# Performance work log

Measured on AMD Instinct MI355X. Metric: run time of the kernel, lower is better.

## Reference

```python
import jax, jax.numpy as jnp
import numpy as np

N_NODES = 100000
N_EDGES = 800000
DIM = 128
BN_EPS = 1e-5


def setup_inputs() -> dict:
    key = jax.random.key(0)
    k1, k2, k3 = jax.random.split(key, 3)
    x = jax.random.normal(k1, (N_NODES, DIM), dtype=jnp.float32)
    edge_index = jax.random.randint(k2, (2, N_EDGES), 0, N_NODES, dtype=jnp.int64)
    # xavier-uniform-like init for the linear weight [out, in]
    limit = float(np.sqrt(6.0 / (DIM + DIM)))
    W = jax.random.uniform(k3, (DIM, DIM), dtype=jnp.float32, minval=-limit, maxval=limit)
    bias = jnp.zeros((DIM,), dtype=jnp.float32)
    bn_gamma = jnp.ones((DIM,), dtype=jnp.float32)
    bn_beta = jnp.zeros((DIM,), dtype=jnp.float32)
    return {"x": x, "edge_index": edge_index, "W": W, "bias": bias,
            "bn_gamma": bn_gamma, "bn_beta": bn_beta, "bit_sum": 0}


def reference(x, edge_index, W, bias, bn_gamma, bn_beta, bit_sum):
    n = x.shape[0]
    # Linear (no bias), is_q=False path; q_xw treated as identity.
    h = x @ W.T                                   # [N, D]
    row, col = edge_index[0], edge_index[1]
    # symmetric degree normalization: deg computed over destination (col)
    deg = jax.ops.segment_sum(jnp.ones_like(col, dtype=h.dtype), col, num_segments=n)
    deg_inv_sqrt = jnp.where(deg > 0, jax.lax.rsqrt(jnp.maximum(deg, 1.0)), 0.0)
    norm = deg_inv_sqrt[row] * deg_inv_sqrt[col]  # [E]
    # message: norm * x_j (x_j = h[row]), aggregate (add) at col
    msg = norm[:, None] * h[row]                  # [E, D]
    out = jax.ops.segment_sum(msg, col, num_segments=n)  # [N, D]
    out = out + bias
    # BatchNorm1d (training mode: batch stats, biased variance)
    mean = jnp.mean(out, axis=0)
    var = jnp.var(out, axis=0)
    out = (out - mean) * jax.lax.rsqrt(var + BN_EPS) * bn_gamma + bn_beta
    # activation
    out = jax.nn.relu(out)
    # residual (in_dim == out_dim); dropout p=0 -> identity
    out = out + x
    return (out, 0)
```

## Files before the change

### kernel.cpp

```cpp
#include <hip/hip_runtime.h>
#include <cstddef>

#define NN 100000
#define DD 128
#define ND (NN * DD)
#define BN_EPS 1e-5f
#define LDA 136
#define NREP 16
#define NBKT 98
#define EPB 4096
#define NT ((NN + 63) / 64)

typedef __bf16 bf16_t;
typedef bf16_t bf16x8 __attribute__((ext_vector_type(8)));
typedef float f32x4 __attribute__((ext_vector_type(4)));
typedef unsigned int uint;
typedef unsigned short ushort;


__device__ __forceinline__ ushort f2b(float f) {
    uint u = __builtin_bit_cast(uint, f);
    u += 0x7FFFu + ((u >> 16) & 1u);
    return (ushort)(u >> 16);
}
__device__ __forceinline__ float b2f(uint s) {
    return __builtin_bit_cast(float, s << 16);
}
__device__ __forceinline__ float blo(uint u) {
    return __builtin_bit_cast(float, u << 16);
}
__device__ __forceinline__ float bhi(uint u) {
    return __builtin_bit_cast(float, u & 0xFFFF0000u);
}

__device__ __forceinline__ int detect_i64(const int* __restrict__ ei) {
    __shared__ int sflag;
    int t = threadIdx.x;
    if (t < 64) {
        int hi = ei[2 * t + 1];
        unsigned long long b = __ballot(hi == 0);
        if (t == 0) sflag = (b == ~0ull) ? 1 : 0;
    }
    __syncthreads();
    return sflag;
}

__global__ __launch_bounds__(256) void k_prep(const int* __restrict__ ei,
                                              int* __restrict__ bktot, int E, int nbh,
                                              const float* __restrict__ x,
                                              uint* __restrict__ xb,
                                              const float* __restrict__ W,
                                              uint* __restrict__ wb) {
    if ((int)blockIdx.x < nbh) {
        int f = detect_i64(ei);
        __shared__ int hist[NBKT];
        int t = threadIdx.x;
        if (t < NBKT) hist[t] = 0;
        __syncthreads();
        int base = blockIdx.x * EPB;
        int count = min(EPB, E - base);
        for (int i = t; i < count; i += 256) {
            int e = base + i;
            int c = f ? ei[2 * (E + e)] : ei[E + e];
            atomicAdd(&hist[c >> 10], 1);
        }
        __syncthreads();
        if (t < NBKT && hist[t] > 0) atomicAdd(&bktot[t], hist[t]);
        return;
    }
    int i = (blockIdx.x - nbh) * 256 + threadIdx.x;
    const float* src;
    uint* dst;
    int j;
    if (i < ND / 8) { src = x; dst = xb; j = i; }
    else { j = i - ND / 8; if (j >= (DD * DD) / 8) return; src = W; dst = wb; }
    const float4* s4 = (const float4*)src;
    float4 a = s4[2 * j], b = s4[2 * j + 1];
    uint4 o;
    o.x = (uint)f2b(a.x) | ((uint)f2b(a.y) << 16);
    o.y = (uint)f2b(a.z) | ((uint)f2b(a.w) << 16);
    o.z = (uint)f2b(b.x) | ((uint)f2b(b.y) << 16);
    o.w = (uint)f2b(b.z) | ((uint)f2b(b.w) << 16);
    ((uint4*)dst)[j] = o;
}

__global__ __launch_bounds__(256) void k_bin(const int* __restrict__ ei,
                                             const int* __restrict__ bktot,
                                             int* __restrict__ bcur,
                                             uint2* __restrict__ pairs, int E) {
    int f = detect_i64(ei);
    __shared__ int bb[NBKT], hist[NBKT], scur[NBKT];
    int t = threadIdx.x;
    if (t < NBKT) { bb[t] = bktot[t]; hist[t] = 0; }
    __syncthreads();
    if (t == 0) {
        int run = 0;
        for (int i = 0; i < NBKT; ++i) { int v = bb[i]; bb[i] = run; run += v; }
    }
    int base = blockIdx.x * EPB;
    int count = min(EPB, E - base);
    int rr[16], cc[16];
#pragma unroll
    for (int k = 0; k < 16; ++k) {
        int i = t + k * 256;
        if (i < count) {
            int e = base + i;
            int r, c;
            if (f) { r = ei[2 * e]; c = ei[2 * (E + e)]; }
            else   { r = ei[e];     c = ei[E + e]; }
            rr[k] = r; cc[k] = c;
            atomicAdd(&hist[c >> 10], 1);
        }
    }
    __syncthreads();
    if (t < NBKT) scur[t] = bb[t] + atomicAdd(&bcur[t], hist[t]);
    __syncthreads();
#pragma unroll
    for (int k = 0; k < 16; ++k) {
        int i = t + k * 256;
        if (i < count) {
            int b = cc[k] >> 10;
            int pos = atomicAdd(&scur[b], 1);
            pairs[pos] = (uint2){(uint)rr[k], (uint)cc[k]};
        }
    }
}

__global__ __launch_bounds__(256) void k_cnt(const uint2* __restrict__ pairs,
                                             const int* __restrict__ bktot,
                                             int* __restrict__ ptr0,
                                             int* __restrict__ cnt,
                                             float* __restrict__ dinv,
                                             int* __restrict__ srow) {
    __shared__ int hist[1024];
    __shared__ int scur[1024];
    __shared__ int ls[256];
    __shared__ int bb[NBKT];
    __shared__ int se0, se1;
    int b = blockIdx.x;
    int t = threadIdx.x;
    if (t < NBKT) bb[t] = bktot[t];
#pragma unroll
    for (int i = 0; i < 4; ++i) hist[t + i * 256] = 0;
    __syncthreads();
    if (t == 0) {
        int run = 0;
        for (int i = 0; i < b; ++i) run += bb[i];
        se0 = run; se1 = run + bb[b];
    }
    __syncthreads();
    int e0 = se0, e1 = se1;
    int nodebase = b << 10;
    for (int i = e0 + t; i < e1; i += 256)
        atomicAdd(&hist[(int)pairs[i].y - nodebase], 1);
    __syncthreads();
    int c4[4];
    int lsum = 0;
#pragma unroll
    for (int i = 0; i < 4; ++i) { c4[i] = hist[t * 4 + i]; lsum += c4[i]; }
    ls[t] = lsum;
    __syncthreads();
    for (int o = 1; o < 256; o <<= 1) {
        int v = (t >= o) ? ls[t - o] : 0;
        __syncthreads();
        ls[t] += v;
        __syncthreads();
    }
    int run = ls[t] - lsum + e0;
#pragma unroll
    for (int i = 0; i < 4; ++i) {
        int idx = nodebase + t * 4 + i;
        if (idx < NN) {
            ptr0[idx] = run;
            cnt[idx] = c4[i];
            dinv[idx] = c4[i] > 0 ? rsqrtf((float)c4[i]) : 0.f;
        }
        scur[t * 4 + i] = run;
        run += c4[i];
    }
    __syncthreads();
    for (int i = e0 + t; i < e1; i += 256) {
        uint2 p = pairs[i];
        int pos = atomicAdd(&scur[(int)p.y - nodebase], 1);
        srow[pos] = (int)p.x;
    }
}

__global__ __launch_bounds__(512, 4) void k_gg(const uint* __restrict__ xb,
                                               const int* __restrict__ srow,
                                               const int* __restrict__ ptr0,
                                               const int* __restrict__ cnt,
                                               const float* __restrict__ dinv,
                                               const ushort* __restrict__ wb,
                                               ushort* __restrict__ hb,
                                               float* __restrict__ csr,
                                               float* __restrict__ cqr) {
    __shared__ ushort sA[64 * LDA];
    __shared__ float cp[8][64], cq[8][64];
    int t = threadIdx.x;
    int wave = t >> 6, lane = t & 63;
    int quad = lane >> 4, l16 = lane & 15;
    uint rowbase = (uint)blockIdx.x * 64;
    const uint4* xb4 = (const uint4*)xb;

    int mn = (int)rowbase + wave * 8 + (lane & 7);
    int sv = 0, kv = 0;
    float dv = 0.f;
    if (lane < 8 && mn < NN) { sv = ptr0[mn]; kv = cnt[mn]; dv = dinv[mn]; }

    for (int bt = 0; bt < 2; ++bt) {
        int ni = bt * 4 + quad;
        int s_here = __shfl(sv, ni);
        int k_here = __shfl(kv, ni);
        float d_here = __shfl(dv, ni);
        int km = max(k_here, __shfl_xor(k_here, 16));
        km = max(km, __shfl_xor(km, 32));

        float ax0 = 0.f, ax1 = 0.f, ax2 = 0.f, ax3 = 0.f;
        float ax4 = 0.f, ax5 = 0.f, ax6 = 0.f, ax7 = 0.f;

        for (int base = 0; base < km; base += 16) {
            int rem = k_here - base;
            int rj = 0;
            if (l16 < rem) rj = srow[s_here + base + l16];
            int jend = km - base; jend = jend > 16 ? 16 : jend;
            for (int j = 0; j < jend; j += 4) {
#pragma unroll
                for (int u = 0; u < 4; ++u) {
                    int jj = j + u;
                    int rsel = __shfl(rj, (lane & 48) + jj);
                    float w = dinv[rsel];
                    uint4 v = xb4[((uint)rsel << 4) + (uint)l16];
                    w = (jj < rem) ? w : 0.f;
                    ax0 = fmaf(w, blo(v.x), ax0); ax1 = fmaf(w, bhi(v.x), ax1);
                    ax2 = fmaf(w, blo(v.y), ax2); ax3 = fmaf(w, bhi(v.y), ax3);
                    ax4 = fmaf(w, blo(v.z), ax4); ax5 = fmaf(w, bhi(v.z), ax5);
                    ax6 = fmaf(w, blo(v.w), ax6); ax7 = fmaf(w, bhi(v.w), ax7);
                }
            }
        }
        uint4 o;
        o.x = (uint)f2b(d_here * ax0) | ((uint)f2b(d_here * ax1) << 16);
        o.y = (uint)f2b(d_here * ax2) | ((uint)f2b(d_here * ax3) << 16);
        o.z = (uint)f2b(d_here * ax4) | ((uint)f2b(d_here * ax5) << 16);
        o.w = (uint)f2b(d_here * ax6) | ((uint)f2b(d_here * ax7) << 16);
        *(uint4*)(sA + (wave * 8 + ni) * LDA + l16 * 8) = o;
    }
    __syncthreads();

    int rg = wave & 3, chh = wave >> 2;
    bf16x8 Af[4];
#pragma unroll
    for (int ks = 0; ks < 4; ++ks)
        Af[ks] = __builtin_bit_cast(
            bf16x8, *(const uint4*)(sA + (rg * 16 + l16) * LDA + ks * 32 + quad * 8));

#pragma unroll
    for (int c = 0; c < 4; ++c) {
        int ctg = chh * 4 + c;
        bf16x8 Bf[4];
#pragma unroll
        for (int ks = 0; ks < 4; ++ks)
            Bf[ks] = __builtin_bit_cast(
                bf16x8,
                *(const uint4*)(wb + (uint)(ctg * 16 + l16) * 128 + ks * 32 + quad * 8));
        f32x4 acc = (f32x4){0.f, 0.f, 0.f, 0.f};
#pragma unroll
        for (int ks = 0; ks < 4; ++ks)
            acc = __builtin_amdgcn_mfma_f32_16x16x32_bf16(Af[ks], Bf[ks], acc, 0, 0, 0);
        float ss = 0.f, qq = 0.f;
#pragma unroll
        for (int r = 0; r < 4; ++r) {
            float v = acc[r];
            ss += v; qq += v * v;
            uint row = rowbase + rg * 16 + quad * 4 + r;
            if (row < NN) hb[row * 128u + (uint)(ctg * 16 + l16)] = f2b(v);
        }
        ss += __shfl_xor(ss, 16); ss += __shfl_xor(ss, 32);
        qq += __shfl_xor(qq, 16); qq += __shfl_xor(qq, 32);
        if (quad == 0) { cp[wave][c * 16 + l16] = ss; cq[wave][c * 16 + l16] = qq; }
    }
    __syncthreads();
    if (t < 128) {
        int w0 = (t >> 6) * 4, lc = t & 63;
        float s = cp[w0][lc] + cp[w0 + 1][lc] + cp[w0 + 2][lc] + cp[w0 + 3][lc];
        float q = cq[w0][lc] + cq[w0 + 1][lc] + cq[w0 + 2][lc] + cq[w0 + 3][lc];
        int rep = ((int)blockIdx.x & (NREP - 1)) * 128 + t;
        atomicAdd(&csr[rep], s);
        atomicAdd(&cqr[rep], q);
    }
}

__global__ __launch_bounds__(256) void k_final(const uint* __restrict__ hb,
                                               const uint* __restrict__ xb,
                                               const float* __restrict__ gamma,
                                               const float* __restrict__ beta,
                                               const float* __restrict__ csr,
                                               const float* __restrict__ cqr,
                                               float* __restrict__ out, int out_size) {
    __shared__ float sa[128], sb[128];
    int t = threadIdx.x;
    const float invN = 1.0f / NN;
    if (t < 128) {
        float s = 0.f;
        for (int i = 0; i < NREP; ++i) s += csr[i * 128 + t];
        sa[t] = s * invN;
    } else {
        int c = t - 128;
        float s = 0.f;
        for (int i = 0; i < NREP; ++i) s += cqr[i * 128 + c];
        sb[c] = s * invN;
    }
    __syncthreads();
    if (t < 128) {
        float m = sa[t];
        float var = sb[t] - m * m;
        float inv = rsqrtf(var + BN_EPS);
        float A = inv * gamma[t];
        float B = beta[t] - m * A;
        sa[t] = A; sb[t] = B;
    }
    __syncthreads();

    int c0 = (t & 7) * 16;
    int u8 = blockIdx.x * 512 + t * 2;
    uint4 hv0 = ((const uint4*)hb)[u8], hv1 = ((const uint4*)hb)[u8 + 1];
    uint4 xv0 = ((const uint4*)xb)[u8], xv1 = ((const uint4*)xb)[u8 + 1];
    uint hu[8] = {hv0.x, hv0.y, hv0.z, hv0.w, hv1.x, hv1.y, hv1.z, hv1.w};
    uint xu[8] = {xv0.x, xv0.y, xv0.z, xv0.w, xv1.x, xv1.y, xv1.z, xv1.w};
    float res[16];
#pragma unroll
    for (int p = 0; p < 8; ++p) {
        int c = c0 + p * 2;
        float h0 = blo(hu[p]), h1 = bhi(hu[p]);
        float x0 = blo(xu[p]), x1 = bhi(xu[p]);
        res[2 * p]     = fmaxf(fmaf(h0, sa[c],     sb[c]),     0.f) + x0;
        res[2 * p + 1] = fmaxf(fmaf(h1, sa[c + 1], sb[c + 1]), 0.f) + x1;
    }
    float4* o4 = (float4*)out;
    int ob = blockIdx.x * 1024 + t * 4;
#pragma unroll
    for (int q = 0; q < 4; ++q)
        o4[ob + q] = (float4){res[4 * q], res[4 * q + 1], res[4 * q + 2], res[4 * q + 3]};
    if (blockIdx.x == 0 && t == 0 && out_size > ND) out[ND] = 0.0f;
}

extern "C" void kernel_launch(void* const* d_in, const int* in_sizes, int n_in,
                              void* d_out, int out_size, void* d_ws, size_t ws_size,
                              hipStream_t stream) {
    const float* x     = (const float*)d_in[0];
    const int*   ei    = (const int*)d_in[1];
    const float* W     = (const float*)d_in[2];
    const float* gamma = (const float*)d_in[4];
    const float* beta  = (const float*)d_in[5];
    float* ws = (float*)d_ws;
    float* out = (float*)d_out;

    uint*   region0  = (uint*)ws;
    uint*   xb       = region0 + ND / 2;
    float*  csr      = (float*)(xb + ND / 2);
    float*  cqr      = csr + NREP * 128;
    int*    bktot    = (int*)(cqr + NREP * 128);
    int*    bcur     = bktot + 128;
    int*    cnt      = bcur + 128;
    int*    ptr0     = cnt + NN;
    float*  dinv     = (float*)(ptr0 + NN);
    int*    srow     = (int*)(dinv + NN);

    int E = in_sizes[1] / 2;
    uint* wb = (uint*)(srow + E);
    uint2* pairs = (uint2*)region0;

    int nbc = (ND / 8 + (DD * DD) / 8 + 255) / 256;
    int nbin = (E + EPB - 1) / EPB;

    hipMemsetAsync(csr, 0, (size_t)(2 * NREP * 128 + 256) * 4, stream);
    k_prep<<<nbin + nbc, 256, 0, stream>>>(ei, bktot, E, nbin, x, xb, W, wb);
    k_bin<<<nbin, 256, 0, stream>>>(ei, bktot, bcur, pairs, E);
    k_cnt<<<NBKT, 256, 0, stream>>>(pairs, bktot, ptr0, cnt, dinv, srow);
    k_gg<<<NT, 512, 0, stream>>>(xb, srow, ptr0, cnt, dinv, (const ushort*)wb,
                                 (ushort*)region0, csr, cqr);
    k_final<<<ND / 4096, 256, 0, stream>>>(region0, xb, gamma, beta, csr, cqr,
                                           out, out_size);
}
```

Measured before the change: 224.0 us.

## Use finer destination buckets and dynamic per-wave node gather in aggregation

Bucket width drops from 1024 to 256 nodes, giving 392 buckets so the counting-sort kernel launches four times as many blocks with one node per thread. The gather stage now has each wave claim whole destination nodes from a shared-memory counter, reading 4 bytes per lane across the full 128-wide row. Edge weights are prefetched per lane and passed by shuffle. The aim is better load balance across waves and more parallelism in the CSR build, at the cost of narrower per-lane loads and an LDS atomic per node.

```diff
diff --git a/kernel.cpp b/kernel.cpp
--- a/kernel.cpp
+++ b/kernel.cpp
@@ -7,7 +7,8 @@
 #define BN_EPS 1e-5f
 #define LDA 136
 #define NREP 16
-#define NBKT 98
+#define NBKT 392
+#define BSH 8
 #define EPB 4096
 #define NT ((NN + 63) / 64)
 
@@ -55,17 +56,18 @@
         int f = detect_i64(ei);
         __shared__ int hist[NBKT];
         int t = threadIdx.x;
-        if (t < NBKT) hist[t] = 0;
+        for (int i = t; i < NBKT; i += 256) hist[i] = 0;
         __syncthreads();
         int base = blockIdx.x * EPB;
         int count = min(EPB, E - base);
         for (int i = t; i < count; i += 256) {
             int e = base + i;
             int c = f ? ei[2 * (E + e)] : ei[E + e];
-            atomicAdd(&hist[c >> 10], 1);
+            atomicAdd(&hist[c >> BSH], 1);
         }
         __syncthreads();
-        if (t < NBKT && hist[t] > 0) atomicAdd(&bktot[t], hist[t]);
+        for (int i = t; i < NBKT; i += 256)
+            if (hist[i] > 0) atomicAdd(&bktot[i], hist[i]);
         return;
     }
     int i = (blockIdx.x - nbh) * 256 + threadIdx.x;
@@ -91,7 +93,7 @@
     int f = detect_i64(ei);
     __shared__ int bb[NBKT], hist[NBKT], scur[NBKT];
     int t = threadIdx.x;
-    if (t < NBKT) { bb[t] = bktot[t]; hist[t] = 0; }
+    for (int i = t; i < NBKT; i += 256) { bb[i] = bktot[i]; hist[i] = 0; }
     __syncthreads();
     if (t == 0) {
         int run = 0;
@@ -109,17 +111,18 @@
             if (f) { r = ei[2 * e]; c = ei[2 * (E + e)]; }
             else   { r = ei[e];     c = ei[E + e]; }
             rr[k] = r; cc[k] = c;
-            atomicAdd(&hist[c >> 10], 1);
-        }
-    }
-    __syncthreads();
-    if (t < NBKT) scur[t] = bb[t] + atomicAdd(&bcur[t], hist[t]);
+            atomicAdd(&hist[c >> BSH], 1);
+        }
+    }
+    __syncthreads();
+    for (int i = t; i < NBKT; i += 256)
+        if (hist[i] > 0) scur[i] = bb[i] + atomicAdd(&bcur[i], hist[i]);
     __syncthreads();
 #pragma unroll
     for (int k = 0; k < 16; ++k) {
         int i = t + k * 256;
         if (i < count) {
-            int b = cc[k] >> 10;
+            int b = cc[k] >> BSH;
             int pos = atomicAdd(&scur[b], 1);
             pairs[pos] = (uint2){(uint)rr[k], (uint)cc[k]};
         }
@@ -132,33 +135,27 @@
                                              int* __restrict__ cnt,
                                              float* __restrict__ dinv,
                                              int* __restrict__ srow) {
-    __shared__ int hist[1024];
-    __shared__ int scur[1024];
-    __shared__ int ls[256];
-    __shared__ int bb[NBKT];
+    __shared__ int sbt[NBKT];
+    __shared__ int hist[256], scur[256], ls[256];
     __shared__ int se0, se1;
     int b = blockIdx.x;
     int t = threadIdx.x;
-    if (t < NBKT) bb[t] = bktot[t];
-#pragma unroll
-    for (int i = 0; i < 4; ++i) hist[t + i * 256] = 0;
+    for (int i = t; i < NBKT; i += 256) sbt[i] = bktot[i];
+    hist[t] = 0;
     __syncthreads();
     if (t == 0) {
         int run = 0;
-        for (int i = 0; i < b; ++i) run += bb[i];
-        se0 = run; se1 = run + bb[b];
+        for (int i = 0; i < b; ++i) run += sbt[i];
+        se0 = run; se1 = run + sbt[b];
     }
     __syncthreads();
     int e0 = se0, e1 = se1;
-    int nodebase = b << 10;
+    int nodebase = b << BSH;
     for (int i = e0 + t; i < e1; i += 256)
         atomicAdd(&hist[(int)pairs[i].y - nodebase], 1);
     __syncthreads();
-    int c4[4];
-    int lsum = 0;
-#pragma unroll
-    for (int i = 0; i < 4; ++i) { c4[i] = hist[t * 4 + i]; lsum += c4[i]; }
-    ls[t] = lsum;
+    int c1 = hist[t];
+    ls[t] = c1;
     __syncthreads();
     for (int o = 1; o < 256; o <<= 1) {
         int v = (t >= o) ? ls[t - o] : 0;
@@ -166,18 +163,14 @@
         ls[t] += v;
         __syncthreads();
     }
-    int run = ls[t] - lsum + e0;
-#pragma unroll
-    for (int i = 0; i < 4; ++i) {
-        int idx = nodebase + t * 4 + i;
-        if (idx < NN) {
-            ptr0[idx] = run;
-            cnt[idx] = c4[i];
-            dinv[idx] = c4[i] > 0 ? rsqrtf((float)c4[i]) : 0.f;
-        }
-        scur[t * 4 + i] = run;
-        run += c4[i];
-    }
+    int run = ls[t] - c1 + e0;
+    int idx = nodebase + t;
+    if (idx < NN) {
+        ptr0[idx] = run;
+        cnt[idx] = c1;
+        dinv[idx] = c1 > 0 ? rsqrtf((float)c1) : 0.f;
+    }
+    scur[t] = run;
     __syncthreads();
     for (int i = e0 + t; i < e1; i += 256) {
         uint2 p = pairs[i];
@@ -197,54 +190,61 @@
                                                float* __restrict__ cqr) {
     __shared__ ushort sA[64 * LDA];
     __shared__ float cp[8][64], cq[8][64];
+    __shared__ int sS[64], sK[64];
+    __shared__ float sD[64];
+    __shared__ int qctr;
     int t = threadIdx.x;
     int wave = t >> 6, lane = t & 63;
     int quad = lane >> 4, l16 = lane & 15;
     uint rowbase = (uint)blockIdx.x * 64;
-    const uint4* xb4 = (const uint4*)xb;
-
-    int mn = (int)rowbase + wave * 8 + (lane & 7);
-    int sv = 0, kv = 0;
-    float dv = 0.f;
-    if (lane < 8 && mn < NN) { sv = ptr0[mn]; kv = cnt[mn]; dv = dinv[mn]; }
-
-    for (int bt = 0; bt < 2; ++bt) {
-        int ni = bt * 4 + quad;
-        int s_here = __shfl(sv, ni);
-        int k_here = __shfl(kv, ni);
-        float d_here = __shfl(dv, ni);
-        int km = max(k_here, __shfl_xor(k_here, 16));
-        km = max(km, __shfl_xor(km, 32));
-
-        float ax0 = 0.f, ax1 = 0.f, ax2 = 0.f, ax3 = 0.f;
-        float ax4 = 0.f, ax5 = 0.f, ax6 = 0.f, ax7 = 0.f;
-
-        for (int base = 0; base < km; base += 16) {
-            int rem = k_here - base;
-            int rj = 0;
-            if (l16 < rem) rj = srow[s_here + base + l16];
-            int jend = km - base; jend = jend > 16 ? 16 : jend;
-            for (int j = 0; j < jend; j += 4) {
-#pragma unroll
-                for (int u = 0; u < 4; ++u) {
-                    int jj = j + u;
-                    int rsel = __shfl(rj, (lane & 48) + jj);
-                    float w = dinv[rsel];
-                    uint4 v = xb4[((uint)rsel << 4) + (uint)l16];
-                    w = (jj < rem) ? w : 0.f;
-                    ax0 = fmaf(w, blo(v.x), ax0); ax1 = fmaf(w, bhi(v.x), ax1);
-                    ax2 = fmaf(w, blo(v.y), ax2); ax3 = fmaf(w, bhi(v.y), ax3);
-                    ax4 = fmaf(w, blo(v.z), ax4); ax5 = fmaf(w, bhi(v.z), ax5);
-                    ax6 = fmaf(w, blo(v.w), ax6); ax7 = fmaf(w, bhi(v.w), ax7);
-                }
+
+    if (t == 0) qctr = 0;
+    if (t < 64) {
+        int node = (int)rowbase + t;
+        bool v = node < NN;
+        sS[t] = v ? ptr0[node] : 0;
+        sK[t] = v ? cnt[node] : 0;
+        sD[t] = v ? dinv[node] : 0.f;
+    }
+    __syncthreads();
+
+    for (;;) {
+        int nl = 0;
+        if (lane == 0) nl = atomicAdd(&qctr, 1);
+        int ni = __shfl(nl, 0);
+        if (ni >= 64) break;
+        int s = sS[ni], k = sK[ni];
+        float dc = sD[ni];
+        float ax = 0.f, ay = 0.f;
+        for (int base = 0; base < k; base += 64) {
+            int m = min(k - base, 64);
+            int rj = 0; float wj = 0.f;
+            if (lane < m) { rj = srow[s + base + lane]; wj = dinv[rj]; }
+            int j = 0;
+            for (; j + 4 <= m; j += 4) {
+                int r0 = __shfl(rj, j);     float w0 = __shfl(wj, j);
+                int r1 = __shfl(rj, j + 1); float w1 = __shfl(wj, j + 1);
+                int r2 = __shfl(rj, j + 2); float w2 = __shfl(wj, j + 2);
+                int r3 = __shfl(rj, j + 3); float w3 = __shfl(wj, j + 3);
+                uint v0 = xb[((uint)r0 << 6) + (uint)lane];
+                uint v1 = xb[((uint)r1 << 6) + (uint)lane];
+                uint v2 = xb[((uint)r2 << 6) + (uint)lane];
+                uint v3 = xb[((uint)r3 << 6) + (uint)lane];
+                ax = fmaf(w0, blo(v0), ax); ay = fmaf(w0, bhi(v0), ay);
+                ax = fmaf(w1, blo(v1), ax); ay = fmaf(w1, bhi(v1), ay);
+                ax = fmaf(w2, blo(v2), ax); ay = fmaf(w2, bhi(v2), ay);
+                ax = fmaf(w3, blo(v3), ax); ay = fmaf(w3, bhi(v3), ay);
             }
-        }
-        uint4 o;
-        o.x = (uint)f2b(d_here * ax0) | ((uint)f2b(d_here * ax1) << 16);
-        o.y = (uint)f2b(d_here * ax2) | ((uint)f2b(d_here * ax3) << 16);
-        o.z = (uint)f2b(d_here * ax4) | ((uint)f2b(d_here * ax5) << 16);
-        o.w = (uint)f2b(d_here * ax6) | ((uint)f2b(d_here * ax7) << 16);
-        *(uint4*)(sA + (wave * 8 + ni) * LDA + l16 * 8) = o;
+            for (; j < m; ++j) {
+                int r = __shfl(rj, j);
+                float w = __shfl(wj, j);
+                uint v = xb[((uint)r << 6) + (uint)lane];
+                ax = fmaf(w, blo(v), ax);
+                ay = fmaf(w, bhi(v), ay);
+            }
+        }
+        *(uint*)(sA + ni * LDA + lane * 2) =
+            (uint)f2b(dc * ax) | ((uint)f2b(dc * ay) << 16);
     }
     __syncthreads();
 
@@ -361,8 +361,8 @@
     float*  csr      = (float*)(xb + ND / 2);
     float*  cqr      = csr + NREP * 128;
     int*    bktot    = (int*)(cqr + NREP * 128);
-    int*    bcur     = bktot + 128;
-    int*    cnt      = bcur + 128;
+    int*    bcur     = bktot + 512;
+    int*    cnt      = bcur + 512;
     int*    ptr0     = cnt + NN;
     float*  dinv     = (float*)(ptr0 + NN);
     int*    srow     = (int*)(dinv + NN);
@@ -374,7 +374,7 @@
     int nbc = (ND / 8 + (DD * DD) / 8 + 255) / 256;
     int nbin = (E + EPB - 1) / EPB;
 
-    hipMemsetAsync(csr, 0, (size_t)(2 * NREP * 128 + 256) * 4, stream);
+    hipMemsetAsync(csr, 0, (size_t)(2 * NREP * 128 + 1024) * 4, stream);
     k_prep<<<nbin + nbc, 256, 0, stream>>>(ei, bktot, E, nbin, x, xb, W, wb);
     k_bin<<<nbin, 256, 0, stream>>>(ei, bktot, bcur, pairs, E);
     k_cnt<<<NBKT, 256, 0, stream>>>(pairs, bktot, ptr0, cnt, dinv, srow);
```

Result: slower. 231.8 us (+3.5%).
